# Performance work log

Hardware: AMD Instinct MI355X
Metric: run time of the kernel (lower is better)

The kernel has to match this reference:

```python
import jax, jax.numpy as jnp
import numpy as np

N_HEAD = 16

def _phi(x):
    # silu(x) + 1 feature map
    return jax.nn.silu(x) + 1.0

def setup_inputs() -> dict:
    key = jax.random.key(0)
    ks = jax.random.split(key, 8)
    B, T, D = 8, 4096, 1024
    s = 0.02
    return {
        "x":  jax.random.normal(ks[0], (B, T, D), jnp.float32),
        "Wq": jax.random.normal(ks[1], (D, D), jnp.float32) * s,
        "bq": jax.random.normal(ks[2], (D,), jnp.float32) * s,
        "Wk": jax.random.normal(ks[3], (D, D), jnp.float32) * s,
        "Wv": jax.random.normal(ks[4], (D, D), jnp.float32) * s,
        "bv": jax.random.normal(ks[5], (D,), jnp.float32) * s,
        "Wo": jax.random.normal(ks[6], (D, D), jnp.float32) * s,
        "bo": jax.random.normal(ks[7], (D,), jnp.float32) * s,
    }

def reference(x, Wq, bq, Wk, Wv, bv, Wo, bo):
    B, T, D = x.shape
    H = N_HEAD
    Dh = D // H
    scale = Dh ** (-0.25)
    # projections (torch F.linear: x @ W.T + b); key has no bias
    q = x @ Wq.T + bq
    k = x @ Wk.T
    v = x @ Wv.T + bv
    # [B, T, H, Dh] -> [B, H, T, Dh]
    q = q.reshape(B, T, H, Dh).transpose(0, 2, 1, 3) * scale
    k = k.reshape(B, T, H, Dh).transpose(0, 2, 1, 3) * scale
    v = v.reshape(B, T, H, Dh).transpose(0, 2, 1, 3)
    phi_q = _phi(q)
    phi_k = _phi(k)
    # kv: [B, H, Dh, Dh] = sum_t phi_k[t]^T v[t]
    kv = jnp.einsum('bhtd,bhte->bhde', phi_k, v)
    out = jnp.einsum('bhtd,bhde->bhte', phi_q, kv)  # [B, H, T, Dh]
    wv = out.transpose(0, 2, 1, 3).reshape(B, T, D)
    return wv @ Wo.T + bo
```

## Files before the change

kernel.cpp:

```cpp
#include <hip/hip_runtime.h>
#include <math.h>

typedef short bf16x8 __attribute__((ext_vector_type(8)));
typedef float f32x4  __attribute__((ext_vector_type(4)));

__device__ __forceinline__ float phi_act(float t) {
    return t / (1.0f + __expf(-t)) + 1.0f;
}

__device__ __forceinline__ unsigned short f2bf(float f) {
    union { float f; unsigned int u; } un; un.f = f;
    unsigned int r = un.u + 0x7fffu + ((un.u >> 16) & 1u);
    return (unsigned short)(r >> 16);
}

__device__ __forceinline__ void gload_lds16(const void* g, void* l) {
    __builtin_amdgcn_global_load_lds(
        (const __attribute__((address_space(1))) void*)g,
        (__attribute__((address_space(3))) void*)l, 16, 0, 0);
}


__device__ __forceinline__ void stage2(const char* g, int voff0, int voff1,
                                       char* l, int wb16) {
    gload_lds16(g + voff0, l + wb16);
    gload_lds16(g + voff1, l + 8192 + wb16);
}

#define LOAD_AF(buf, ah) do {                                                   \
    const char* _s = (const char*)&As[buf][ah][0];                              \
    _Pragma("unroll")                                                           \
    for (int _mi = 0; _mi < 4; _mi++) {                                         \
        const int _row = qm * 64 + _mi * 16 + ml;                               \
        const int _sw = (_row & 7) << 4;                                        \
        _Pragma("unroll")                                                       \
        for (int _ks = 0; _ks < 2; _ks++)                                       \
            af[_mi][_ks] = *(const bf16x8*)(_s +                                \
                (((_row * 128) + _ks * 64 + kq * 16) ^ _sw));                   \
    }                                                                           \
} while (0)

#define LOAD_BF_TO(dst, buf, bh) do {                                           \
    const char* _s = (const char*)&Bs[buf][bh][0];                              \
    _Pragma("unroll")                                                           \
    for (int _nj = 0; _nj < 2; _nj++) {                                         \
        const int _col = qn * 32 + _nj * 16 + ml;                               \
        const int _sw = (_col & 7) << 4;                                        \
        _Pragma("unroll")                                                       \
        for (int _ks = 0; _ks < 2; _ks++)                                       \
            dst[_nj][_ks] = *(const bf16x8*)(_s +                               \
                (((_col * 128) + _ks * 64 + kq * 16) ^ _sw));                   \
    }                                                                           \
} while (0)

#define MFMA_Q(Q, B) do {                                                       \
    __builtin_amdgcn_s_setprio(1);                                              \
    _Pragma("unroll")                                                           \
    for (int _mi = 0; _mi < 4; _mi++)                                           \
        _Pragma("unroll")                                                       \
        for (int _nj = 0; _nj < 2; _nj++)                                       \
            _Pragma("unroll")                                                   \
            for (int _ks = 0; _ks < 2; _ks++)                                   \
                acc[Q][_mi][_nj] = __builtin_amdgcn_mfma_f32_16x16x32_bf16(     \
                    af[_mi][_ks], B[_nj][_ks], acc[Q][_mi][_nj], 0, 0, 0);      \
    __builtin_amdgcn_s_setprio(0);                                              \
} while (0)

template<int KIND>
__device__ __forceinline__ void gemm256_body(
    const unsigned short* __restrict__ A, const unsigned short* __restrict__ W,
    const float* __restrict__ bq, const float* __restrict__ bv,
    unsigned short* __restrict__ oq, unsigned short* __restrict__ okk,
    unsigned short* __restrict__ ov, float* __restrict__ outF,
    const float* __restrict__ bo, float scale, int NBN)
{
    __shared__ __align__(128) unsigned short As[2][2][128 * 64];
    __shared__ __align__(128) unsigned short Bs[2][2][128 * 64];

    const int tid  = threadIdx.x;
    const int lane = tid & 63;
    const int w    = tid >> 6;
    const int qm   = w >> 2;
    const int qn   = w & 3;
    const int ml   = lane & 15;
    const int kq   = lane >> 4;

    const int nwg  = (int)gridDim.x;
    const int bid  = (int)blockIdx.x;
    const int sbid = (bid & 7) * (nwg >> 3) + (bid >> 3);
    const int bn   = sbid % NBN;
    const int bm   = sbid / NBN;

    const char* pA = (const char*)(A + (size_t)bm * 256 * 1024);
    const char* pB = (const char*)(W + (size_t)bn * 256 * 1024);

    int voff[2];
    #pragma unroll
    for (int u = 0; u < 2; u++) {
        const int p  = (u * 512 + tid) * 16;
        const int qq = p ^ (((p >> 7) & 7) << 4);
        voff[u] = (qq >> 7) * 2048 + (qq & 127);
    }
    const int wb16 = (tid & ~63) * 16;

    f32x4 acc[4][4][2];
    f32x4 zero4 = {0.f, 0.f, 0.f, 0.f};
    #pragma unroll
    for (int q = 0; q < 4; q++)
        #pragma unroll
        for (int mi = 0; mi < 4; mi++)
            #pragma unroll
            for (int nj = 0; nj < 2; nj++) acc[q][mi][nj] = zero4;

    bf16x8 af[4][2], bf0[2][2], bf1[2][2];

    stage2(pA,              voff[0], voff[1], (char*)&As[0][0][0], wb16);
    stage2(pB,              voff[0], voff[1], (char*)&Bs[0][0][0], wb16);
    stage2(pB + 256 * 1024, voff[0], voff[1], (char*)&Bs[0][1][0], wb16);
    stage2(pA + 256 * 1024, voff[0], voff[1], (char*)&As[0][1][0], wb16);

    for (int t = 0; t < 16; ++t) {
        const int buf = t & 1;
        const char* A0n = pA + (size_t)(t + 1) * 128;
        const char* A1n = A0n + 256 * 1024;
        const char* B0n = pB + (size_t)(t + 1) * 128;
        const char* B1n = B0n + 256 * 1024;
        const bool st = (t + 1 < 16);

        asm volatile("s_waitcnt vmcnt(4)" ::: "memory");
        __builtin_amdgcn_s_barrier();
        asm volatile("" ::: "memory");
        LOAD_AF(buf, 0);
        LOAD_BF_TO(bf0, buf, 0);
        if (st) {
            stage2(A0n, voff[0], voff[1], (char*)&As[buf ^ 1][0][0], wb16);
            stage2(B0n, voff[0], voff[1], (char*)&Bs[buf ^ 1][0][0], wb16);
        }
        asm volatile("s_waitcnt lgkmcnt(0)" ::: "memory");
        MFMA_Q(0, bf0);

        if (st) { asm volatile("s_waitcnt vmcnt(6)" ::: "memory"); }
        else    { asm volatile("s_waitcnt vmcnt(2)" ::: "memory"); }
        __builtin_amdgcn_s_barrier();
        asm volatile("" ::: "memory");
        LOAD_BF_TO(bf1, buf, 1);
        if (st) stage2(B1n, voff[0], voff[1], (char*)&Bs[buf ^ 1][1][0], wb16);
        asm volatile("s_waitcnt lgkmcnt(0)" ::: "memory");
        MFMA_Q(1, bf1);

        if (st) { asm volatile("s_waitcnt vmcnt(6)" ::: "memory"); }
        else    { asm volatile("s_waitcnt vmcnt(0)" ::: "memory"); }
        __builtin_amdgcn_s_barrier();
        asm volatile("" ::: "memory");
        LOAD_AF(buf, 1);
        if (st) stage2(A1n, voff[0], voff[1], (char*)&As[buf ^ 1][1][0], wb16);
        asm volatile("s_waitcnt lgkmcnt(0)" ::: "memory");
        MFMA_Q(2, bf1);

        MFMA_Q(3, bf0);
    }

    const int rq = lane >> 4, cl = lane & 15;
    #pragma unroll
    for (int q = 0; q < 4; q++) {
        const int qr = (q >> 1) * 128;
        const int qc = ((q == 1) || (q == 2)) ? 128 : 0;
        #pragma unroll
        for (int nj = 0; nj < 2; nj++) {
            const int colg = bn * 256 + qc + qn * 32 + nj * 16 + cl;
            if constexpr (KIND == 0) {
                const int z    = colg >> 10;
                const int lcol = colg & 1023;
                const float bias = (z == 0) ? bq[lcol] : ((z == 2) ? bv[lcol] : 0.f);
                unsigned short* dst = (z == 0) ? oq : ((z == 1) ? okk : ov);
                #pragma unroll
                for (int mi = 0; mi < 4; mi++) {
                    const int row0 = bm * 256 + qr + qm * 64 + mi * 16 + rq * 4;
                    #pragma unroll
                    for (int r = 0; r < 4; r++) {
                        float vv = acc[q][mi][nj][r] + bias;
                        if (z < 2) vv = phi_act(vv * scale);
                        dst[(size_t)(row0 + r) * 1024 + lcol] = f2bf(vv);
                    }
                }
            } else {
                const float bias = bo[colg];
                #pragma unroll
                for (int mi = 0; mi < 4; mi++) {
                    const int row0 = bm * 256 + qr + qm * 64 + mi * 16 + rq * 4;
                    #pragma unroll
                    for (int r = 0; r < 4; r++)
                        outF[(size_t)(row0 + r) * 1024 + colg] = acc[q][mi][nj][r] + bias;
                }
            }
        }
    }
}

__global__ __launch_bounds__(512, 2) void qkv_gemm256(
    const unsigned short* __restrict__ xb,
    const unsigned short* __restrict__ wcat,
    const float* __restrict__ bq, const float* __restrict__ bv,
    unsigned short* __restrict__ phiq, unsigned short* __restrict__ phik,
    unsigned short* __restrict__ vb, float scale)
{
    gemm256_body<0>(xb, wcat, bq, bv, phiq, phik, vb, nullptr, nullptr, scale, 12);
}

__global__ __launch_bounds__(512, 2) void out_gemm256(
    const unsigned short* __restrict__ A, const unsigned short* __restrict__ W,
    const float* __restrict__ bo, float* __restrict__ out)
{
    gemm256_body<1>(A, W, nullptr, nullptr, nullptr, nullptr, nullptr, out, bo, 1.0f, 4);
}

__global__ __launch_bounds__(256) void cast_all(
    const float* __restrict__ x,  unsigned short* __restrict__ xb,
    const float* __restrict__ w0, unsigned short* __restrict__ w0b,
    const float* __restrict__ w1, unsigned short* __restrict__ w1b,
    const float* __restrict__ w2, unsigned short* __restrict__ w2b,
    const float* __restrict__ w3, unsigned short* __restrict__ w3b,
    size_t nx, size_t nw)
{
    size_t i = ((size_t)blockIdx.x * 256 + threadIdx.x) * 4;
    const float* s; unsigned short* d; size_t off;
    if (i < nx)               { s = x;  d = xb;  off = i; }
    else if (i < nx + nw)     { s = w0; d = w0b; off = i - nx; }
    else if (i < nx + 2 * nw) { s = w1; d = w1b; off = i - nx - nw; }
    else if (i < nx + 3 * nw) { s = w2; d = w2b; off = i - nx - 2 * nw; }
    else                      { s = w3; d = w3b; off = i - nx - 3 * nw; }
    float4 v = *(const float4*)(s + off);
    ushort4 o;
    o.x = f2bf(v.x); o.y = f2bf(v.y); o.z = f2bf(v.z); o.w = f2bf(v.w);
    *(ushort4*)(d + off) = o;
}

__global__ __launch_bounds__(256) void kv_part(
    const unsigned short* __restrict__ phiK, const unsigned short* __restrict__ V,
    float* __restrict__ partial, int Ttot, int D)
{
    const int tc = blockIdx.x, bh = blockIdx.y;
    const int b = bh >> 4, h = bh & 15;
    const int tbase = tc * 512;

    __shared__ unsigned short pkT[64][72];
    __shared__ unsigned short vvT[64][72];

    const int tid  = threadIdx.x;
    const int lane = tid & 63;
    const int w    = tid >> 6;
    const int dq = w >> 1, eq = w & 1;
    const int kq = lane >> 4, ml = lane & 15;

    f32x4 zero4 = {0.f, 0.f, 0.f, 0.f};
    f32x4 acc[2][2];
    acc[0][0] = zero4; acc[0][1] = zero4; acc[1][0] = zero4; acc[1][1] = zero4;

    const size_t base = (size_t)b * Ttot * D + h * 64;

    for (int c8 = 0; c8 < 8; c8++) {
        const int t0 = tbase + c8 * 64;
        __syncthreads();
        #pragma unroll
        for (int u = 0; u < 2; u++) {
            const int f = tid * 2 + u;
            const int trow = f >> 3;
            const int d8 = (f & 7) * 8;
            const int tw = trow ^ ((d8 >> 3) << 3);
            const size_t g = base + (size_t)(t0 + trow) * D + d8;
            uint4 kk = *(const uint4*)(phiK + g);
            uint4 vv = *(const uint4*)(V + g);
            pkT[d8 + 0][tw] = (unsigned short)(kk.x & 0xffff);
            pkT[d8 + 1][tw] = (unsigned short)(kk.x >> 16);
            pkT[d8 + 2][tw] = (unsigned short)(kk.y & 0xffff);
            pkT[d8 + 3][tw] = (unsigned short)(kk.y >> 16);
            pkT[d8 + 4][tw] = (unsigned short)(kk.z & 0xffff);
            pkT[d8 + 5][tw] = (unsigned short)(kk.z >> 16);
            pkT[d8 + 6][tw] = (unsigned short)(kk.w & 0xffff);
            pkT[d8 + 7][tw] = (unsigned short)(kk.w >> 16);
            vvT[d8 + 0][tw] = (unsigned short)(vv.x & 0xffff);
            vvT[d8 + 1][tw] = (unsigned short)(vv.x >> 16);
            vvT[d8 + 2][tw] = (unsigned short)(vv.y & 0xffff);
            vvT[d8 + 3][tw] = (unsigned short)(vv.y >> 16);
            vvT[d8 + 4][tw] = (unsigned short)(vv.z & 0xffff);
            vvT[d8 + 5][tw] = (unsigned short)(vv.z >> 16);
            vvT[d8 + 6][tw] = (unsigned short)(vv.w & 0xffff);
            vvT[d8 + 7][tw] = (unsigned short)(vv.w >> 16);
        }
        __syncthreads();

        #pragma unroll
        for (int ks = 0; ks < 2; ks++) {
            bf16x8 af[2], bfv[2];
            #pragma unroll
            for (int ai = 0; ai < 2; ai++) {
                const int row = dq * 32 + ai * 16 + ml;
                const int col = ((ks * 4 + kq) ^ ((row >> 3) & 7)) << 3;
                af[ai] = *(const bf16x8*)&pkT[row][col];
            }
            #pragma unroll
            for (int bi = 0; bi < 2; bi++) {
                const int row = eq * 32 + bi * 16 + ml;
                const int col = ((ks * 4 + kq) ^ ((row >> 3) & 7)) << 3;
                bfv[bi] = *(const bf16x8*)&vvT[row][col];
            }
            #pragma unroll
            for (int ai = 0; ai < 2; ai++)
                #pragma unroll
                for (int bi = 0; bi < 2; bi++)
                    acc[ai][bi] = __builtin_amdgcn_mfma_f32_16x16x32_bf16(
                        af[ai], bfv[bi], acc[ai][bi], 0, 0, 0);
        }
    }

    float* outp = partial + ((size_t)bh * 8 + tc) * 4096;
    const int rq = lane >> 4, cl = lane & 15;
    #pragma unroll
    for (int ai = 0; ai < 2; ai++)
        #pragma unroll
        for (int bi = 0; bi < 2; bi++) {
            const int e = eq * 32 + bi * 16 + cl;
            #pragma unroll
            for (int r = 0; r < 4; r++) {
                const int d = dq * 32 + ai * 16 + rq * 4 + r;
                outp[d * 64 + e] = acc[ai][bi][r];
            }
        }
}

__global__ __launch_bounds__(256) void kv_reduce(
    const float* __restrict__ partial, unsigned short* __restrict__ kvT)
{
    const int bh = blockIdx.x;
    const int tid = threadIdx.x;
    __shared__ float s[64][65];
    float a[16];
    #pragma unroll
    for (int c = 0; c < 16; c++) a[c] = 0.f;
    #pragma unroll
    for (int p = 0; p < 8; p++) {
        const float* src = partial + ((size_t)bh * 8 + p) * 4096;
        #pragma unroll
        for (int c = 0; c < 16; c++) a[c] += src[c * 256 + tid];
    }
    #pragma unroll
    for (int c = 0; c < 16; c++) {
        const int idx = c * 256 + tid;
        s[idx >> 6][idx & 63] = a[c];
    }
    __syncthreads();
    unsigned short* outp = kvT + (size_t)bh * 4096;
    #pragma unroll
    for (int c = 0; c < 16; c++) {
        const int j = c * 256 + tid;
        outp[j] = f2bf(s[j & 63][j >> 6]);
    }
}

__global__ __launch_bounds__(256) void av_mfma(
    const unsigned short* __restrict__ phiQ, const unsigned short* __restrict__ kvT,
    unsigned short* __restrict__ Oattn, int Ttot, int D)
{
    const int bh = blockIdx.y;
    const int b = bh >> 4, h = bh & 15;
    const int t0 = blockIdx.x * 256;

    __shared__ unsigned short Aq[256 * 64];
    __shared__ unsigned short Kv[64][72];

    const int tid  = threadIdx.x;
    const int lane = tid & 63;
    const int w    = tid >> 6;
    const int kq = lane >> 4, ml = lane & 15;

    {
        const int e = tid >> 2;
        const int c16 = (tid & 3) * 16;
        const unsigned short* src = kvT + (size_t)bh * 4096 + e * 64 + c16;
        *(uint4*)&Kv[e][c16]     = *(const uint4*)(src);
        *(uint4*)&Kv[e][c16 + 8] = *(const uint4*)(src + 8);
    }
    {
        const int lr = lane >> 3;
        const int d8 = (lane & 7) * 8;
        #pragma unroll
        for (int r = 0; r < 8; r++) {
            const int chunk = r * 4 + w;
            const int row = chunk * 8 + lr;
            gload_lds16(phiQ + ((size_t)(b * Ttot + t0 + row)) * D + h * 64 + d8,
                        &Aq[chunk * 512]);
        }
    }
    __syncthreads();

    f32x4 zero4 = {0.f, 0.f, 0.f, 0.f};
    f32x4 acc[4][4];
    #pragma unroll
    for (int i = 0; i < 4; i++)
        #pragma unroll
        for (int j = 0; j < 4; j++) acc[i][j] = zero4;

    #pragma unroll
    for (int ks = 0; ks < 2; ks++) {
        bf16x8 af[4], bfv[4];
        #pragma unroll
        for (int mi = 0; mi < 4; mi++)
            af[mi] = *(const bf16x8*)&Aq[(w * 64 + mi * 16 + ml) * 64 + ks * 32 + kq * 8];
        #pragma unroll
        for (int nj = 0; nj < 4; nj++)
            bfv[nj] = *(const bf16x8*)&Kv[nj * 16 + ml][ks * 32 + kq * 8];
        #pragma unroll
        for (int mi = 0; mi < 4; mi++)
            #pragma unroll
            for (int nj = 0; nj < 4; nj++)
                acc[mi][nj] = __builtin_amdgcn_mfma_f32_16x16x32_bf16(
                    af[mi], bfv[nj], acc[mi][nj], 0, 0, 0);
    }

    const int rq = lane >> 4, cl = lane & 15;
    #pragma unroll
    for (int mi = 0; mi < 4; mi++) {
        #pragma unroll
        for (int r = 0; r < 4; r++) {
            const int t = t0 + w * 64 + mi * 16 + rq * 4 + r;
            unsigned short* dst = Oattn + (size_t)(b * Ttot + t) * D + h * 64;
            #pragma unroll
            for (int nj = 0; nj < 4; nj++)
                dst[nj * 16 + cl] = f2bf(acc[mi][nj][r]);
        }
    }
}

extern "C" void kernel_launch(void* const* d_in, const int* in_sizes, int n_in,
                              void* d_out, int out_size, void* d_ws, size_t ws_size,
                              hipStream_t stream) {
    const float* x  = (const float*)d_in[0];
    const float* Wq = (const float*)d_in[1];
    const float* bq = (const float*)d_in[2];
    const float* Wk = (const float*)d_in[3];
    const float* Wv = (const float*)d_in[4];
    const float* bv = (const float*)d_in[5];
    const float* Wo = (const float*)d_in[6];
    const float* bo = (const float*)d_in[7];
    float* out = (float*)d_out;

    const int B = 8, T = 4096, D = 1024;
    const int M = B * T;
    const float scale = 0.35355339059327379f;
    const size_t MD = (size_t)M * D;
    const size_t WN = (size_t)D * D;

    unsigned short* xb    = (unsigned short*)d_ws;
    unsigned short* wqb   = xb + MD;
    unsigned short* wkb   = wqb + WN;
    unsigned short* wvb   = wkb + WN;
    unsigned short* wob   = wvb + WN;
    unsigned short* phiq  = wob + WN;
    unsigned short* phik  = phiq + MD;
    unsigned short* vb    = phik + MD;
    unsigned short* oat   = vb + MD;
    float*          part  = (float*)(oat + MD);
    unsigned short* kvT   = (unsigned short*)(part + (size_t)1024 * 4096);
    (void)ws_size; (void)in_sizes; (void)n_in; (void)out_size;

    dim3 blk(256);

    {
        size_t total4 = (MD + 4 * WN) / 4;
        cast_all<<<dim3((unsigned)(total4 / 256)), blk, 0, stream>>>(
            x, xb, Wq, wqb, Wk, wkb, Wv, wvb, Wo, wob, MD, WN);
    }

    qkv_gemm256<<<dim3(1536), dim3(512), 0, stream>>>(
        xb, wqb, bq, bv, phiq, phik, vb, scale);

    kv_part<<<dim3(8, 128), blk, 0, stream>>>(phik, vb, part, T, D);
    kv_reduce<<<dim3(128), blk, 0, stream>>>(part, kvT);

    av_mfma<<<dim3(T / 256, 128), blk, 0, stream>>>(phiq, kvT, oat, T, D);

    out_gemm256<<<dim3(512), dim3(512), 0, stream>>>(oat, wob, bo, out);
}
```

Measured before the change: 607.5 us.

## Fold per-head kv into output projection weights, drop attention-output pass

Instead of computing phi_q·kv into an intermediate attention output and then multiplying by Wo, each batch gets an effective weight Weff[b] = Wo·blockdiag(kv_h). The output GEMM then reads phi_q directly with a per-batch weight selected by row block. This removes the av kernel and the write and read of a full-size intermediate activation, at the cost of a small per-batch weight GEMM and an extra bf16 rounding of the combined weights. The kv_part LDS transpose is also rewritten to pack two tokens per 32-bit store, reducing the number of shared-memory writes.

```diff
diff --git a/kernel.cpp b/kernel.cpp
--- a/kernel.cpp
+++ b/kernel.cpp
@@ -92,7 +92,9 @@
     const int bm   = sbid / NBN;
 
     const char* pA = (const char*)(A + (size_t)bm * 256 * 1024);
-    const char* pB = (const char*)(W + (size_t)bn * 256 * 1024);
+    const unsigned short* Wbase =
+        (KIND == 1) ? (W + (size_t)(bm >> 4) * 1024 * 1024) : W;
+    const char* pB = (const char*)(Wbase + (size_t)bn * 256 * 1024);
 
     int voff[2];
     #pragma unroll
@@ -252,40 +254,34 @@
     const int dq = w >> 1, eq = w & 1;
     const int kq = lane >> 4, ml = lane & 15;
 
+    const int tq  = tid >> 3;
+    const int oct = tid & 7;
+    const int d8  = oct * 8;
+    const int tw0 = (tq * 2) ^ (oct << 3);
+
     f32x4 zero4 = {0.f, 0.f, 0.f, 0.f};
     f32x4 acc[2][2];
     acc[0][0] = zero4; acc[0][1] = zero4; acc[1][0] = zero4; acc[1][1] = zero4;
 
     const size_t base = (size_t)b * Ttot * D + h * 64;
 
+#define PACKW(arr, lo, hi, i0)                                                   \
+    *(unsigned int*)&arr[d8 + i0    ][tw0] = ((lo) & 0xffffu) | ((hi) << 16);    \
+    *(unsigned int*)&arr[d8 + i0 + 1][tw0] = ((lo) >> 16) | ((hi) & 0xffff0000u);
+
     for (int c8 = 0; c8 < 8; c8++) {
         const int t0 = tbase + c8 * 64;
         __syncthreads();
-        #pragma unroll
-        for (int u = 0; u < 2; u++) {
-            const int f = tid * 2 + u;
-            const int trow = f >> 3;
-            const int d8 = (f & 7) * 8;
-            const int tw = trow ^ ((d8 >> 3) << 3);
-            const size_t g = base + (size_t)(t0 + trow) * D + d8;
-            uint4 kk = *(const uint4*)(phiK + g);
-            uint4 vv = *(const uint4*)(V + g);
-            pkT[d8 + 0][tw] = (unsigned short)(kk.x & 0xffff);
-            pkT[d8 + 1][tw] = (unsigned short)(kk.x >> 16);
-            pkT[d8 + 2][tw] = (unsigned short)(kk.y & 0xffff);
-            pkT[d8 + 3][tw] = (unsigned short)(kk.y >> 16);
-            pkT[d8 + 4][tw] = (unsigned short)(kk.z & 0xffff);
-            pkT[d8 + 5][tw] = (unsigned short)(kk.z >> 16);
-            pkT[d8 + 6][tw] = (unsigned short)(kk.w & 0xffff);
-            pkT[d8 + 7][tw] = (unsigned short)(kk.w >> 16);
-            vvT[d8 + 0][tw] = (unsigned short)(vv.x & 0xffff);
-            vvT[d8 + 1][tw] = (unsigned short)(vv.x >> 16);
-            vvT[d8 + 2][tw] = (unsigned short)(vv.y & 0xffff);
-            vvT[d8 + 3][tw] = (unsigned short)(vv.y >> 16);
-            vvT[d8 + 4][tw] = (unsigned short)(vv.z & 0xffff);
-            vvT[d8 + 5][tw] = (unsigned short)(vv.z >> 16);
-            vvT[d8 + 6][tw] = (unsigned short)(vv.w & 0xffff);
-            vvT[d8 + 7][tw] = (unsigned short)(vv.w >> 16);
+        {
+            const size_t g0 = base + (size_t)(t0 + tq * 2) * D + d8;
+            uint4 k0 = *(const uint4*)(phiK + g0);
+            uint4 k1 = *(const uint4*)(phiK + g0 + D);
+            uint4 v0 = *(const uint4*)(V + g0);
+            uint4 v1 = *(const uint4*)(V + g0 + D);
+            PACKW(pkT, k0.x, k1.x, 0) PACKW(pkT, k0.y, k1.y, 2)
+            PACKW(pkT, k0.z, k1.z, 4) PACKW(pkT, k0.w, k1.w, 6)
+            PACKW(vvT, v0.x, v1.x, 0) PACKW(vvT, v0.y, v1.y, 2)
+            PACKW(vvT, v0.z, v1.z, 4) PACKW(vvT, v0.w, v1.w, 6)
         }
         __syncthreads();
 
@@ -312,6 +308,7 @@
                         af[ai], bfv[bi], acc[ai][bi], 0, 0, 0);
         }
     }
+#undef PACKW
 
     float* outp = partial + ((size_t)bh * 8 + tc) * 4096;
     const int rq = lane >> 4, cl = lane & 15;
@@ -328,106 +325,103 @@
         }
 }
 
-__global__ __launch_bounds__(256) void kv_reduce(
-    const float* __restrict__ partial, unsigned short* __restrict__ kvT)
+__global__ __launch_bounds__(256) void kv_weff(
+    const float* __restrict__ partial, const unsigned short* __restrict__ wob,
+    unsigned short* __restrict__ weff)
 {
     const int bh = blockIdx.x;
-    const int tid = threadIdx.x;
-    __shared__ float s[64][65];
-    float a[16];
-    #pragma unroll
-    for (int c = 0; c < 16; c++) a[c] = 0.f;
-    #pragma unroll
-    for (int p = 0; p < 8; p++) {
-        const float* src = partial + ((size_t)bh * 8 + p) * 4096;
-        #pragma unroll
-        for (int c = 0; c < 16; c++) a[c] += src[c * 256 + tid];
-    }
-    #pragma unroll
-    for (int c = 0; c < 16; c++) {
-        const int idx = c * 256 + tid;
-        s[idx >> 6][idx & 63] = a[c];
-    }
-    __syncthreads();
-    unsigned short* outp = kvT + (size_t)bh * 4096;
-    #pragma unroll
-    for (int c = 0; c < 16; c++) {
-        const int j = c * 256 + tid;
-        outp[j] = f2bf(s[j & 63][j >> 6]);
-    }
-}
-
-__global__ __launch_bounds__(256) void av_mfma(
-    const unsigned short* __restrict__ phiQ, const unsigned short* __restrict__ kvT,
-    unsigned short* __restrict__ Oattn, int Ttot, int D)
-{
-    const int bh = blockIdx.y;
     const int b = bh >> 4, h = bh & 15;
-    const int t0 = blockIdx.x * 256;
-
-    __shared__ unsigned short Aq[256 * 64];
-    __shared__ unsigned short Kv[64][72];
+
+    __shared__ unsigned short kvs[64][72];
+    __shared__ __align__(128) unsigned short Awo[128 * 64];
 
     const int tid  = threadIdx.x;
     const int lane = tid & 63;
     const int w    = tid >> 6;
-    const int kq = lane >> 4, ml = lane & 15;
+    const int ml = lane & 15, kq = lane >> 4;
 
     {
-        const int e = tid >> 2;
-        const int c16 = (tid & 3) * 16;
-        const unsigned short* src = kvT + (size_t)bh * 4096 + e * 64 + c16;
-        *(uint4*)&Kv[e][c16]     = *(const uint4*)(src);
-        *(uint4*)&Kv[e][c16 + 8] = *(const uint4*)(src + 8);
-    }
-    {
-        const int lr = lane >> 3;
-        const int d8 = (lane & 7) * 8;
-        #pragma unroll
-        for (int r = 0; r < 8; r++) {
-            const int chunk = r * 4 + w;
-            const int row = chunk * 8 + lr;
-            gload_lds16(phiQ + ((size_t)(b * Ttot + t0 + row)) * D + h * 64 + d8,
-                        &Aq[chunk * 512]);
+        float a[16];
+        #pragma unroll
+        for (int c = 0; c < 16; c++) a[c] = 0.f;
+        #pragma unroll
+        for (int p = 0; p < 8; p++) {
+            const float* src = partial + ((size_t)bh * 8 + p) * 4096;
+            #pragma unroll
+            for (int c = 0; c < 16; c++) a[c] += src[c * 256 + tid];
+        }
+        #pragma unroll
+        for (int c = 0; c < 16; c++) {
+            const int idx = c * 256 + tid;
+            kvs[idx >> 6][idx & 63] = f2bf(a[c]);
         }
     }
     __syncthreads();
 
-    f32x4 zero4 = {0.f, 0.f, 0.f, 0.f};
-    f32x4 acc[4][4];
-    #pragma unroll
-    for (int i = 0; i < 4; i++)
-        #pragma unroll
-        for (int j = 0; j < 4; j++) acc[i][j] = zero4;
-
-    #pragma unroll
-    for (int ks = 0; ks < 2; ks++) {
-        bf16x8 af[4], bfv[4];
-        #pragma unroll
-        for (int mi = 0; mi < 4; mi++)
-            af[mi] = *(const bf16x8*)&Aq[(w * 64 + mi * 16 + ml) * 64 + ks * 32 + kq * 8];
-        #pragma unroll
-        for (int nj = 0; nj < 4; nj++)
-            bfv[nj] = *(const bf16x8*)&Kv[nj * 16 + ml][ks * 32 + kq * 8];
-        #pragma unroll
-        for (int mi = 0; mi < 4; mi++)
+    bf16x8 bfv[4][2];
+    #pragma unroll
+    for (int nj = 0; nj < 4; nj++)
+        #pragma unroll
+        for (int ks = 0; ks < 2; ks++)
+            bfv[nj][ks] = *(const bf16x8*)&kvs[nj * 16 + ml][ks * 32 + kq * 8];
+
+    int voff[4];
+    #pragma unroll
+    for (int u = 0; u < 4; u++) {
+        const int p  = (u * 256 + tid) * 16;
+        const int qq = p ^ (((p >> 7) & 7) << 4);
+        voff[u] = (qq >> 7) * 2048 + (qq & 127);
+    }
+    const int wb = tid & ~63;
+    const char* gsrc = (const char*)wob + (size_t)h * 128;
+    unsigned short* dstb = weff + (size_t)b * 1024 * 1024 + h * 64;
+    const int rq = lane >> 4, cl = lane & 15;
+
+    for (int oc = 0; oc < 8; ++oc) {
+        __syncthreads();
+        #pragma unroll
+        for (int u = 0; u < 4; u++)
+            gload_lds16(gsrc + (size_t)oc * 128 * 2048 + voff[u],
+                        (char*)Awo + (size_t)(u * 256 + wb) * 16);
+        asm volatile("s_waitcnt vmcnt(0)" ::: "memory");
+        __syncthreads();
+
+        bf16x8 af[2][2];
+        #pragma unroll
+        for (int mi = 0; mi < 2; mi++) {
+            const int r128 = w * 32 + mi * 16 + ml;
+            const int sw = (r128 & 7) << 4;
+            #pragma unroll
+            for (int ks = 0; ks < 2; ks++)
+                af[mi][ks] = *(const bf16x8*)((const char*)Awo +
+                    (((r128 * 128) + ks * 64 + kq * 16) ^ sw));
+        }
+
+        f32x4 acc[2][4];
+        f32x4 zero4 = {0.f, 0.f, 0.f, 0.f};
+        #pragma unroll
+        for (int mi = 0; mi < 2; mi++)
+            #pragma unroll
+            for (int nj = 0; nj < 4; nj++) acc[mi][nj] = zero4;
+
+        #pragma unroll
+        for (int ks = 0; ks < 2; ks++)
+            #pragma unroll
+            for (int mi = 0; mi < 2; mi++)
+                #pragma unroll
+                for (int nj = 0; nj < 4; nj++)
+                    acc[mi][nj] = __builtin_amdgcn_mfma_f32_16x16x32_bf16(
+                        af[mi][ks], bfv[nj][ks], acc[mi][nj], 0, 0, 0);
+
+        #pragma unroll
+        for (int mi = 0; mi < 2; mi++)
             #pragma unroll
             for (int nj = 0; nj < 4; nj++)
-                acc[mi][nj] = __builtin_amdgcn_mfma_f32_16x16x32_bf16(
-                    af[mi], bfv[nj], acc[mi][nj], 0, 0, 0);
-    }
-
-    const int rq = lane >> 4, cl = lane & 15;
-    #pragma unroll
-    for (int mi = 0; mi < 4; mi++) {
-        #pragma unroll
-        for (int r = 0; r < 4; r++) {
-            const int t = t0 + w * 64 + mi * 16 + rq * 4 + r;
-            unsigned short* dst = Oattn + (size_t)(b * Ttot + t) * D + h * 64;
-            #pragma unroll
-            for (int nj = 0; nj < 4; nj++)
-                dst[nj * 16 + cl] = f2bf(acc[mi][nj][r]);
-        }
+                #pragma unroll
+                for (int r = 0; r < 4; r++) {
+                    const int o = oc * 128 + w * 32 + mi * 16 + rq * 4 + r;
+                    dstb[(size_t)o * 1024 + nj * 16 + cl] = f2bf(acc[mi][nj][r]);
+                }
     }
 }
 
@@ -458,9 +452,8 @@
     unsigned short* phiq  = wob + WN;
     unsigned short* phik  = phiq + MD;
     unsigned short* vb    = phik + MD;
-    unsigned short* oat   = vb + MD;
-    float*          part  = (float*)(oat + MD);
-    unsigned short* kvT   = (unsigned short*)(part + (size_t)1024 * 4096);
+    unsigned short* weff  = vb + MD;
+    float*          part  = (float*)(weff + (size_t)8 * 1024 * 1024);
     (void)ws_size; (void)in_sizes; (void)n_in; (void)out_size;
 
     dim3 blk(256);
@@ -475,9 +468,7 @@
         xb, wqb, bq, bv, phiq, phik, vb, scale);
 
     kv_part<<<dim3(8, 128), blk, 0, stream>>>(phik, vb, part, T, D);
-    kv_reduce<<<dim3(128), blk, 0, stream>>>(part, kvT);
-
-    av_mfma<<<dim3(T / 256, 128), blk, 0, stream>>>(phiq, kvT, oat, T, D);
-
-    out_gemm256<<<dim3(512), dim3(512), 0, stream>>>(oat, wob, bo, out);
-}
+    kv_weff<<<dim3(128), blk, 0, stream>>>(part, wob, weff);
+
+    out_gemm256<<<dim3(512), dim3(512), 0, stream>>>(phiq, weff, bo, out);
+}
```

Measured after the change: 584.7 us. 1.04x faster.
